# Kernel optimization log

Hardware: AMD Instinct MI355X
Metric: run time of the kernel (lower is better)

## Reference

```python
import jax, jax.numpy as jnp
import numpy as np

E = 8      # n_routed_experts
TOPK = 2
D = 768    # hidden_dim
F = 3072   # routed_expert_inter_dim (== shared_expert_inter_dim)


def setup_inputs() -> dict:
    key = jax.random.key(0)
    ks = jax.random.split(key, 11)
    s = 0.02
    return {
        "x": jax.random.normal(ks[0], (2, 64, 64, D), dtype=jnp.float32),
        "gate_w": jax.random.normal(ks[1], (E, D), dtype=jnp.float32),          # Gate.weight (torch randn init)
        "w1": jax.random.normal(ks[2], (E, F, D), dtype=jnp.float32) * s,       # Expert.fc1.weight per expert
        "b1": jax.random.normal(ks[3], (E, F), dtype=jnp.float32) * s,
        "w2": jax.random.normal(ks[4], (E, D, F), dtype=jnp.float32) * s,       # Expert.fc2.weight per expert
        "b2": jax.random.normal(ks[5], (E, D), dtype=jnp.float32) * s,
        "ws1": jax.random.normal(ks[6], (F, D), dtype=jnp.float32) * s,         # shared GeluMLP fc1
        "bs1": jax.random.normal(ks[7], (F,), dtype=jnp.float32) * s,
        "ws2": jax.random.normal(ks[8], (D, F), dtype=jnp.float32) * s,         # shared GeluMLP fc2
        "bs2": jax.random.normal(ks[9], (D,), dtype=jnp.float32) * s,
    }


def _gelu(v):
    return jax.nn.gelu(v, approximate=False)  # torch nn.GELU default = exact erf


def reference(x, gate_w, w1, b1, w2, b2, ws1, bs1, ws2, bs2):
    B, H, W, Dh = x.shape
    xf = x.reshape(-1, Dh)                                  # [T, D]
    T = xf.shape[0]

    # Gate: softmax over expert logits, top-k, renormalize
    scores = jax.nn.softmax(xf @ gate_w.T, axis=-1)         # [T, E]
    vals, idx = jax.lax.top_k(scores, TOPK)                 # [T, K]
    vals = vals / jnp.sum(vals, axis=-1, keepdims=True)

    # Dense combine weights: 0 for unselected experts (faithful to scatter-add)
    cw = jnp.zeros((T, E), dtype=xf.dtype).at[
        jnp.arange(T)[:, None], idx
    ].add(vals)                                             # [T, E]

    # Routed experts: small fixed structural loop over E experts
    out = jnp.zeros_like(xf)
    for e in range(E):
        h = _gelu(xf @ w1[e].T + b1[e])                     # [T, F]
        y = h @ w2[e].T + b2[e]                             # [T, D]
        out = out + y * cw[:, e:e + 1]

    # Shared expert (GeluMLP) applied to all tokens
    shared = _gelu(xf @ ws1.T + bs1) @ ws2.T + bs2          # [T, D]

    return (out + shared).reshape(B, H, W, Dh)
```

## Files before the change

### kernel.cpp

```cpp
#include <hip/hip_runtime.h>
#include <hip/hip_bf16.h>

#define T_TOK 8192
#define E_EXP 8
#define DDIM  768
#define FDIM  3072

typedef _Float16 f16x8 __attribute__((ext_vector_type(8)));
typedef _Float16 f16x4 __attribute__((ext_vector_type(4)));
typedef float    f32x4 __attribute__((ext_vector_type(4)));

static const size_t XH_OFF   = 0;
static const size_t W1H_OFF  = 12582912;
static const size_t Y_OFF    = W1H_OFF;
static const size_t W2H_OFF  = 50331648;
static const size_t WS1H_OFF = 88080384;
static const size_t WS2H_OFF = 92798976;
static const size_t H_OFF    = 97517568;
static const size_t ROWS_OFF = 198180864;
static const size_t RW_OFF   = 198246400;
static const size_t TIDX_OFF = 198311936;
static const size_t TW_OFF   = 198377472;
static const size_t CNT_OFF  = 198443008;
static const size_t BASE_OFF = 198443264;
static const size_t CUR_OFF  = 198443520;
static const size_t TSLOT_OFF= 198443776;
static const size_t WS_NEED  = 198509312;

__global__ void cvt_f32_f16(const float* __restrict__ src, _Float16* __restrict__ dst, int n4) {
    int i = blockIdx.x * blockDim.x + threadIdx.x;
    if (i >= n4) return;
    float4 v = ((const float4*)src)[i];
    f16x4 o = { (_Float16)v.x, (_Float16)v.y, (_Float16)v.z, (_Float16)v.w };
    *(f16x4*)(dst + 4 * (size_t)i) = o;
}

__global__ void gate_kernel(const float* __restrict__ x, const float* __restrict__ gw,
                            int* __restrict__ tidx, float* __restrict__ tw) {
    int wave = threadIdx.x >> 6;
    int lane = threadIdx.x & 63;
    int t = blockIdx.x * 4 + wave;
    const float4* xv = (const float4*)(x + (size_t)t * DDIM);
    float p[E_EXP];
#pragma unroll
    for (int e = 0; e < E_EXP; e++) p[e] = 0.f;
    for (int i = lane; i < DDIM / 4; i += 64) {
        float4 xv4 = xv[i];
#pragma unroll
        for (int e = 0; e < E_EXP; e++) {
            float4 g = ((const float4*)(gw + (size_t)e * DDIM))[i];
            p[e] += xv4.x * g.x + xv4.y * g.y + xv4.z * g.z + xv4.w * g.w;
        }
    }
#pragma unroll
    for (int e = 0; e < E_EXP; e++) {
#pragma unroll
        for (int off = 32; off; off >>= 1) p[e] += __shfl_xor(p[e], off);
    }
    if (lane == 0) {
        int i0 = 0;
#pragma unroll
        for (int e = 1; e < E_EXP; e++) if (p[e] > p[i0]) i0 = e;
        int i1 = (i0 == 0) ? 1 : 0;
#pragma unroll
        for (int e = 0; e < E_EXP; e++) {
            if (e == i0) continue;
            if (p[e] > p[i1]) i1 = e;
        }
        float d  = p[i1] - p[i0];
        float e1 = expf(d);
        float w0 = 1.f / (1.f + e1);
        float w1 = 1.f - w0;
        tidx[2 * t]     = i0;  tw[2 * t]     = w0;
        tidx[2 * t + 1] = i1;  tw[2 * t + 1] = w1;
    }
}

__global__ void count_kernel(const int* __restrict__ tidx, int* __restrict__ cnt,
                             int* __restrict__ base, int* __restrict__ cur) {
    int c[E_EXP];
#pragma unroll
    for (int e = 0; e < E_EXP; e++) c[e] = 0;
    for (int i = threadIdx.x; i < 2 * T_TOK; i += 1024) {
        int e = tidx[i];
#pragma unroll
        for (int k = 0; k < E_EXP; k++) c[k] += (e == k) ? 1 : 0;
    }
#pragma unroll
    for (int e = 0; e < E_EXP; e++) {
#pragma unroll
        for (int off = 32; off; off >>= 1) c[e] += __shfl_xor(c[e], off);
    }
    __shared__ int wsum[16][E_EXP];
    int lane = threadIdx.x & 63, wave = threadIdx.x >> 6;
    if (lane == 0) {
#pragma unroll
        for (int e = 0; e < E_EXP; e++) wsum[wave][e] = c[e];
    }
    __syncthreads();
    if (threadIdx.x == 0) {
        int acc = 0;
        for (int e = 0; e < E_EXP; e++) {
            int s = 0;
            for (int w = 0; w < 16; w++) s += wsum[w][e];
            cnt[e] = s; base[e] = acc; cur[e] = acc; acc += s;
        }
    }
}

__global__ void scatter_kernel(const int* __restrict__ tidx, const float* __restrict__ tw,
                               int* __restrict__ cur, int* __restrict__ rowsIdx,
                               float* __restrict__ rw, int* __restrict__ tslot) {
    int t = blockIdx.x * 256 + threadIdx.x;
    int lane = threadIdx.x & 63, wave = threadIdx.x >> 6;
    unsigned long long lt = ((unsigned long long)1 << lane) - 1ull;
    __shared__ int wcnt[8][E_EXP];
    __shared__ int wpre[8][E_EXP];
    __shared__ int bbase[E_EXP];

    int myE[2], myR[2];
#pragma unroll
    for (int k = 0; k < 2; k++) {
        int e = tidx[2 * t + k];
        myE[k] = e;
        int vw = wave * 2 + k;
        int rank = 0;
#pragma unroll
        for (int ee = 0; ee < E_EXP; ee++) {
            unsigned long long m = __ballot(e == ee);
            if (e == ee) rank = __builtin_popcountll(m & lt);
            if (lane == 0) wcnt[vw][ee] = __builtin_popcountll(m);
        }
        myR[k] = rank;
    }
    __syncthreads();
    if (threadIdx.x < E_EXP) {
        int e = threadIdx.x, acc = 0;
#pragma unroll
        for (int vw = 0; vw < 8; vw++) { wpre[vw][e] = acc; acc += wcnt[vw][e]; }
        bbase[e] = atomicAdd(&cur[e], acc);
    }
    __syncthreads();
#pragma unroll
    for (int k = 0; k < 2; k++) {
        int e = myE[k];
        int slot = bbase[e] + wpre[wave * 2 + k][e] + myR[k];
        rowsIdx[slot] = t;
        rw[slot] = tw[2 * t + k];
        tslot[2 * t + k] = slot;
    }
}

__global__ void combine_kernel(const _Float16* __restrict__ y,
                               const int* __restrict__ tslot,
                               float* __restrict__ out) {
    int idx = blockIdx.x * 256 + threadIdx.x;
    int t = idx / (DDIM / 8);
    int c = (idx % (DDIM / 8)) * 8;
    int s0 = tslot[2 * t], s1 = tslot[2 * t + 1];
    f16x8 a = *(const f16x8*)(y + (size_t)s0 * DDIM + c);
    f16x8 b = *(const f16x8*)(y + (size_t)s1 * DDIM + c);
    float4* o = (float4*)(out + (size_t)t * DDIM + c);
    float4 o0 = o[0], o1 = o[1];
    o0.x += (float)a[0] + (float)b[0];
    o0.y += (float)a[1] + (float)b[1];
    o0.z += (float)a[2] + (float)b[2];
    o0.w += (float)a[3] + (float)b[3];
    o1.x += (float)a[4] + (float)b[4];
    o1.y += (float)a[5] + (float)b[5];
    o1.z += (float)a[6] + (float)b[6];
    o1.w += (float)a[7] + (float)b[7];
    o[0] = o0; o[1] = o1;
}

#define FC1S 0
#define FC2S 1
#define FC1R 2
#define FC2R 3

template <int MODE>
__global__ __launch_bounds__(256, 2) void gemm_kernel(
    const _Float16* __restrict__ Abase,
    const _Float16* __restrict__ Wbase,
    const float* __restrict__ biasBase,
    _Float16* __restrict__ h,
    float* __restrict__ out,
    const int* __restrict__ cnt, const int* __restrict__ base,
    const int* __restrict__ rowsIdx, const float* __restrict__ rw)
{
    constexpr int K = (MODE == FC1S || MODE == FC1R) ? DDIM : FDIM;
    constexpr int N = (MODE == FC1S || MODE == FC1R) ? FDIM : DDIM;
    constexpr bool ROUTED = (MODE == FC1R || MODE == FC2R);

    int m0, mEnd;
    const _Float16* W;
    const float* bias;
    if constexpr (ROUTED) {
        int bx = blockIdx.x, accb = 0, expert = -1, rb = 0;
#pragma unroll
        for (int e = 0; e < E_EXP; e++) {
            int nb = (cnt[e] + 127) >> 7;
            if (expert < 0 && bx < accb + nb) { expert = e; rb = bx - accb; }
            accb += nb;
        }
        if (expert < 0) return;
        m0   = base[expert] + rb * 128;
        mEnd = base[expert] + cnt[expert];
        W    = Wbase + (size_t)expert * N * K;
        bias = biasBase + (size_t)expert * N;
    } else {
        m0 = blockIdx.x * 128;
        mEnd = T_TOK;
        W = Wbase;
        bias = biasBase;
    }
    int n0 = blockIdx.y * 128;

    __shared__ __align__(16) _Float16 As[128 * 72];
    __shared__ __align__(16) _Float16 Bs[128 * 72];

    int tid  = threadIdx.x;
    int lane = tid & 63;
    int wid  = tid >> 6;
    int wm   = wid >> 1, wn = wid & 1;
    int m16  = lane & 15, q = lane >> 4;

    f32x4 acc[4][4];
#pragma unroll
    for (int i = 0; i < 4; i++)
#pragma unroll
        for (int j = 0; j < 4; j++) acc[i][j] = f32x4{0.f, 0.f, 0.f, 0.f};

    int arowg[4];
#pragma unroll
    for (int tse = 0; tse < 4; tse++) {
        int s = tid + tse * 256;
        int row = s >> 3;
        int pr = m0 + row;
        bool valid = pr < mEnd;
        int ar;
        if constexpr (MODE == FC1R) ar = valid ? rowsIdx[pr] : 0;
        else                        ar = pr;
        arowg[tse] = valid ? ar : -1;
    }

    for (int k0 = 0; k0 < K; k0 += 64) {
#pragma unroll
        for (int tse = 0; tse < 4; tse++) {
            int s = tid + tse * 256;
            int row = s >> 3, cs = s & 7;
            int4 v = make_int4(0, 0, 0, 0);
            int ar = arowg[tse];
            if (ar >= 0) v = *(const int4*)(Abase + (size_t)ar * K + k0 + cs * 8);
            *(int4*)(As + row * 72 + cs * 8) = v;
        }
#pragma unroll
        for (int tse = 0; tse < 4; tse++) {
            int s = tid + tse * 256;
            int row = s >> 3, cs = s & 7;
            int4 v = *(const int4*)(W + (size_t)(n0 + row) * K + k0 + cs * 8);
            *(int4*)(Bs + row * 72 + cs * 8) = v;
        }
        __syncthreads();
#pragma unroll
        for (int ks = 0; ks < 2; ks++) {
            f16x8 af[4], bf[4];
#pragma unroll
            for (int i = 0; i < 4; i++)
                af[i] = *(const f16x8*)(As + (wm * 64 + i * 16 + m16) * 72 + ks * 32 + q * 8);
#pragma unroll
            for (int j = 0; j < 4; j++)
                bf[j] = *(const f16x8*)(Bs + (wn * 64 + j * 16 + m16) * 72 + ks * 32 + q * 8);
#pragma unroll
            for (int i = 0; i < 4; i++)
#pragma unroll
                for (int j = 0; j < 4; j++)
                    acc[i][j] = __builtin_amdgcn_mfma_f32_16x16x32_f16(af[i], bf[j], acc[i][j], 0, 0, 0);
        }
        __syncthreads();
    }

    float biasv[4];
#pragma unroll
    for (int j = 0; j < 4; j++) biasv[j] = bias[n0 + wn * 64 + j * 16 + m16];

#pragma unroll
    for (int i = 0; i < 4; i++) {
#pragma unroll
        for (int r = 0; r < 4; r++) {
            int rowp = m0 + wm * 64 + i * 16 + q * 4 + r;
            if (rowp >= mEnd) continue;
            float wgt = 0.f;
            if constexpr (MODE == FC2R) wgt = rw[rowp];
#pragma unroll
            for (int j = 0; j < 4; j++) {
                int col = n0 + wn * 64 + j * 16 + m16;
                float v = acc[i][j][r] + biasv[j];
                if constexpr (MODE == FC1S || MODE == FC1R) {
                    v = 0.5f * v * (1.f + erff(v * 0.70710678118f));
                    h[(size_t)rowp * FDIM + col] = (_Float16)v;
                } else if constexpr (MODE == FC2S) {
                    out[(size_t)rowp * DDIM + col] = v;
                } else {
                    h[(size_t)rowp * DDIM + col] = (_Float16)(v * wgt);
                }
            }
        }
    }
}

extern "C" void kernel_launch(void* const* d_in, const int* in_sizes, int n_in,
                              void* d_out, int out_size, void* d_ws, size_t ws_size,
                              hipStream_t stream) {
    const float* x   = (const float*)d_in[0];
    const float* gw  = (const float*)d_in[1];
    const float* w1  = (const float*)d_in[2];
    const float* b1  = (const float*)d_in[3];
    const float* w2  = (const float*)d_in[4];
    const float* b2  = (const float*)d_in[5];
    const float* ws1 = (const float*)d_in[6];
    const float* bs1 = (const float*)d_in[7];
    const float* ws2 = (const float*)d_in[8];
    const float* bs2 = (const float*)d_in[9];
    float* out = (float*)d_out;
    char* ws = (char*)d_ws;
    if (ws_size < WS_NEED) return;

    _Float16* xh   = (_Float16*)(ws + XH_OFF);
    _Float16* w1h  = (_Float16*)(ws + W1H_OFF);
    _Float16* yb   = (_Float16*)(ws + Y_OFF);
    _Float16* w2h  = (_Float16*)(ws + W2H_OFF);
    _Float16* ws1h = (_Float16*)(ws + WS1H_OFF);
    _Float16* ws2h = (_Float16*)(ws + WS2H_OFF);
    _Float16* h    = (_Float16*)(ws + H_OFF);
    int*   rowsIdx = (int*)(ws + ROWS_OFF);
    float* rw      = (float*)(ws + RW_OFF);
    int*   tidx    = (int*)(ws + TIDX_OFF);
    float* tw      = (float*)(ws + TW_OFF);
    int*   cnt     = (int*)(ws + CNT_OFF);
    int*   base    = (int*)(ws + BASE_OFF);
    int*   cur     = (int*)(ws + CUR_OFF);
    int*   tslot   = (int*)(ws + TSLOT_OFF);

    cvt_f32_f16<<<6144,  256, 0, stream>>>(x,   xh,   1572864);
    cvt_f32_f16<<<18432, 256, 0, stream>>>(w1,  w1h,  4718592);
    cvt_f32_f16<<<18432, 256, 0, stream>>>(w2,  w2h,  4718592);
    cvt_f32_f16<<<2304,  256, 0, stream>>>(ws1, ws1h, 589824);
    cvt_f32_f16<<<2304,  256, 0, stream>>>(ws2, ws2h, 589824);

    gate_kernel<<<2048, 256, 0, stream>>>(x, gw, tidx, tw);
    count_kernel<<<1, 1024, 0, stream>>>(tidx, cnt, base, cur);
    scatter_kernel<<<32, 256, 0, stream>>>(tidx, tw, cur, rowsIdx, rw, tslot);

    gemm_kernel<FC1S><<<dim3(64, 24),  256, 0, stream>>>(xh, ws1h, bs1, h, out, cnt, base, rowsIdx, rw);
    gemm_kernel<FC2S><<<dim3(64, 6),   256, 0, stream>>>(h,  ws2h, bs2, h, out, cnt, base, rowsIdx, rw);
    gemm_kernel<FC1R><<<dim3(136, 24), 256, 0, stream>>>(xh, w1h,  b1,  h, out, cnt, base, rowsIdx, rw);
    gemm_kernel<FC2R><<<dim3(136, 6),  256, 0, stream>>>(h,  w2h,  b2,  yb, out, cnt, base, rowsIdx, rw);

    combine_kernel<<<3072, 256, 0, stream>>>(yb, tslot, out);
}
```

Baseline: 714.7 us.

## Load GEMM tiles directly into LDS with XOR-swizzled layout

```diff
diff --git a/kernel.cpp b/kernel.cpp
--- a/kernel.cpp
+++ b/kernel.cpp
@@ -216,14 +216,15 @@
     }
     int n0 = blockIdx.y * 128;
 
-    __shared__ __align__(16) _Float16 As[128 * 72];
-    __shared__ __align__(16) _Float16 Bs[128 * 72];
+    __shared__ __align__(16) _Float16 As[128 * 64];
+    __shared__ __align__(16) _Float16 Bs[128 * 64];
 
     int tid  = threadIdx.x;
     int lane = tid & 63;
     int wid  = tid >> 6;
     int wm   = wid >> 1, wn = wid & 1;
     int m16  = lane & 15, q = lane >> 4;
+    int x7   = m16 & 7;
 
     f32x4 acc[4][4];
 #pragma unroll
@@ -231,35 +232,38 @@
 #pragma unroll
         for (int j = 0; j < 4; j++) acc[i][j] = f32x4{0.f, 0.f, 0.f, 0.f};
 
-    int arowg[4];
+    const _Float16* ap[4];
+    const _Float16* bp[4];
 #pragma unroll
     for (int tse = 0; tse < 4; tse++) {
-        int s = tid + tse * 256;
-        int row = s >> 3;
-        int pr = m0 + row;
+        int L = wid * 256 + tse * 64 + lane;
+        int r = L >> 3;
+        int c = (L & 7) ^ (r & 7);
+        int pr = m0 + r;
         bool valid = pr < mEnd;
         int ar;
-        if constexpr (MODE == FC1R) ar = valid ? rowsIdx[pr] : 0;
-        else                        ar = pr;
-        arowg[tse] = valid ? ar : -1;
+        if constexpr (MODE == FC1R) ar = rowsIdx[valid ? pr : m0];
+        else                        ar = valid ? pr : m0;
+        ap[tse] = Abase + (size_t)ar * K + c * 8;
+        bp[tse] = W + (size_t)(n0 + r) * K + c * 8;
     }
 
     for (int k0 = 0; k0 < K; k0 += 64) {
 #pragma unroll
         for (int tse = 0; tse < 4; tse++) {
-            int s = tid + tse * 256;
-            int row = s >> 3, cs = s & 7;
-            int4 v = make_int4(0, 0, 0, 0);
-            int ar = arowg[tse];
-            if (ar >= 0) v = *(const int4*)(Abase + (size_t)ar * K + k0 + cs * 8);
-            *(int4*)(As + row * 72 + cs * 8) = v;
+            __builtin_amdgcn_global_load_lds(
+                (const __attribute__((address_space(1))) void*)ap[tse],
+                (__attribute__((address_space(3))) void*)(As + wid * 2048 + tse * 512),
+                16, 0, 0);
+            ap[tse] += 64;
         }
 #pragma unroll
         for (int tse = 0; tse < 4; tse++) {
-            int s = tid + tse * 256;
-            int row = s >> 3, cs = s & 7;
-            int4 v = *(const int4*)(W + (size_t)(n0 + row) * K + k0 + cs * 8);
-            *(int4*)(Bs + row * 72 + cs * 8) = v;
+            __builtin_amdgcn_global_load_lds(
+                (const __attribute__((address_space(1))) void*)bp[tse],
+                (__attribute__((address_space(3))) void*)(Bs + wid * 2048 + tse * 512),
+                16, 0, 0);
+            bp[tse] += 64;
         }
         __syncthreads();
 #pragma unroll
@@ -267,10 +271,10 @@
             f16x8 af[4], bf[4];
 #pragma unroll
             for (int i = 0; i < 4; i++)
-                af[i] = *(const f16x8*)(As + (wm * 64 + i * 16 + m16) * 72 + ks * 32 + q * 8);
+                af[i] = *(const f16x8*)(As + (wm * 64 + i * 16 + m16) * 64 + (((ks * 4 + q) ^ x7) * 8));
 #pragma unroll
             for (int j = 0; j < 4; j++)
-                bf[j] = *(const f16x8*)(Bs + (wn * 64 + j * 16 + m16) * 72 + ks * 32 + q * 8);
+                bf[j] = *(const f16x8*)(Bs + (wn * 64 + j * 16 + m16) * 64 + (((ks * 4 + q) ^ x7) * 8));
 #pragma unroll
             for (int i = 0; i < 4; i++)
 #pragma unroll
```

Measured after the change: 594.7 us. -16.8%, faster.
